# Kernel optimization log

Measured on AMD Instinct MI355X. Metric: run time of the kernel, lower is better.

## Reference

```python
import jax, jax.numpy as jnp
import numpy as np

XBOUND = (-51.2, 51.2, 0.8)
YBOUND = (-51.2, 51.2, 0.8)
ZBOUND = (-10.0, 10.0, 20.0)
DBOUND = (1.0, 60.0, 1.0)
IMG_H, IMG_W = 256, 704
DOWNSAMPLE = 16
CAM_C = 64
OUT_C = 64
D = int((DBOUND[1] - DBOUND[0]) / DBOUND[2])      # 59
NX = int((XBOUND[1] - XBOUND[0]) / XBOUND[2])     # 128
NY = int((YBOUND[1] - YBOUND[0]) / YBOUND[2])     # 128
NZ = int((ZBOUND[1] - ZBOUND[0]) / ZBOUND[2])     # 1
FH, FW = IMG_H // DOWNSAMPLE, IMG_W // DOWNSAMPLE # 16, 44
DX = jnp.array([XBOUND[2], YBOUND[2], ZBOUND[2]], dtype=jnp.float32)
BX = jnp.array([XBOUND[0] + XBOUND[2] / 2.0, YBOUND[0] + YBOUND[2] / 2.0, ZBOUND[0] + ZBOUND[2] / 2.0], dtype=jnp.float32)


def make_frustum():
    ds = jnp.arange(DBOUND[0], DBOUND[1], DBOUND[2], dtype=jnp.float32)   # [D]
    xs = jnp.linspace(0.0, IMG_W - 1.0, FW, dtype=jnp.float32)            # [FW]
    ys = jnp.linspace(0.0, IMG_H - 1.0, FH, dtype=jnp.float32)            # [FH]
    d = jnp.broadcast_to(ds[:, None, None], (D, FH, FW))
    x = jnp.broadcast_to(xs[None, None, :], (D, FH, FW))
    y = jnp.broadcast_to(ys[None, :, None], (D, FH, FW))
    return jnp.stack([x, y, d], axis=-1)                                  # [D,FH,FW,3]


def get_geometry(rots, trans, intrins, post_rots, post_trans):
    # rots/intrins/post_rots: [B,N,3,3]; trans/post_trans: [B,N,3]
    frustum = make_frustum()                                              # [D,FH,FW,3]
    pts = frustum[None, None] - post_trans[:, :, None, None, None]        # [B,N,D,FH,FW,3]
    pts = jnp.einsum('bnij,bndhwj->bndhwi', jnp.linalg.inv(post_rots), pts)
    pts = jnp.concatenate([pts[..., :2] * pts[..., 2:3], pts[..., 2:3]], axis=-1)
    comb = jnp.matmul(rots, jnp.linalg.inv(intrins))
    pts = jnp.einsum('bnij,bndhwj->bndhwi', comb, pts)
    return pts + trans[:, :, None, None, None]


def forward(x, rots, trans, intrins, post_rots, post_trans, w_depth, b_depth):
    B, N, C_in, H, W = x.shape
    # 1x1 conv == channel matmul
    y = jnp.einsum('bnchw,oc->bnohw', x, w_depth) + b_depth[None, None, :, None, None]
    depth = jax.nn.softmax(y[:, :, :D], axis=2)              # [B,N,D,H,W]
    context = y[:, :, D:]                                    # [B,N,OUT_C,H,W]
    outer = depth[:, :, :, None] * context[:, :, None, :]    # [B,N,D,OUT_C,H,W]
    outer = jnp.transpose(outer, (0, 1, 2, 4, 5, 3))         # [B,N,D,H,W,OUT_C]

    geom = jax.lax.stop_gradient(get_geometry(rots, trans, intrins, post_rots, post_trans))
    # torch .long() truncates toward zero -> jnp.trunc
    g = jnp.trunc((geom.reshape(-1, 3) - (BX - DX / 2.0)) / DX).astype(jnp.int32)  # [P,3]
    kept = ((g[:, 0] >= 0) & (g[:, 0] < NX) &
            (g[:, 1] >= 0) & (g[:, 1] < NY) &
            (g[:, 2] >= 0) & (g[:, 2] < NZ))
    batch_ix = jnp.repeat(jnp.arange(B, dtype=jnp.int32), N * D * H * W)
    ranks = batch_ix * (NX * NY * NZ) + g[:, 0] + g[:, 1] * NX + g[:, 2] * NX * NY
    # segment-sum over voxel ranks == sort+cumsum trick + scatter in the original
    feats = jnp.where(kept[:, None], outer.reshape(-1, OUT_C), 0.0)
    ranks = jnp.where(kept, ranks, 0)
    bev = jax.ops.segment_sum(feats, ranks, num_segments=B * NZ * NY * NX)
    bev = bev.reshape(B, NZ, NY, NX, OUT_C).transpose(0, 4, 1, 2, 3).sum(axis=2)
    return bev  # [B, OUT_C, NY, NX]


def setup_inputs() -> dict:
    key = jax.random.key(0)
    B, N = 4, 6
    ks = jax.random.split(key, 8)
    cam2ego = jnp.array([[0.0, 0.0, 1.0], [-1.0, 0.0, 0.0], [0.0, -1.0, 0.0]], dtype=jnp.float32)
    rots = jnp.broadcast_to(cam2ego, (B, N, 3, 3)) + 0.02 * jax.random.normal(ks[0], (B, N, 3, 3), dtype=jnp.float32)
    trans = 1.0 * jax.random.normal(ks[1], (B, N, 3), dtype=jnp.float32)
    K = jnp.array([[700.0, 0.0, IMG_W / 2.0], [0.0, 700.0, IMG_H / 2.0], [0.0, 0.0, 1.0]], dtype=jnp.float32)
    intrins = jnp.broadcast_to(K, (B, N, 3, 3)) + 0.1 * jax.random.normal(ks[2], (B, N, 3, 3), dtype=jnp.float32)
    post_rots = jnp.broadcast_to(jnp.eye(3, dtype=jnp.float32), (B, N, 3, 3)) + 0.01 * jax.random.normal(ks[3], (B, N, 3, 3), dtype=jnp.float32)
    post_trans = 0.1 * jax.random.normal(ks[4], (B, N, 3), dtype=jnp.float32)
    x = jax.random.normal(ks[5], (B, N, CAM_C, FH, FW), dtype=jnp.float32)
    w_depth = 0.05 * jax.random.normal(ks[6], (D + OUT_C, CAM_C), dtype=jnp.float32)
    b_depth = jnp.zeros((D + OUT_C,), dtype=jnp.float32)
    return {"x": x, "rots": rots, "trans": trans, "intrins": intrins,
            "post_rots": post_rots, "post_trans": post_trans,
            "w_depth": w_depth, "b_depth": b_depth}


def reference(x, rots, trans, intrins, post_rots, post_trans, w_depth, b_depth):
    return forward(x, rots, trans, intrins, post_rots, post_trans, w_depth, b_depth)
```

## Files before the change

kernel.cpp:

```cpp
#include <hip/hip_runtime.h>
#include <math.h>

#define Bc 4
#define Nc 6
#define Dc 59
#define FHc 16
#define FWc 44
#define Cc 64
#define OCc 123
#define NXc 128
#define NYc 128
#define NVOX (Bc*NXc*NYc)
#define NBLK (Bc*Nc*FWc)
#define NBLK2 (NBLK*2)

#define WS_ACC 0
#define WS_CAM ((size_t)16777216)
#define WS_WDT ((size_t)16781312)

template<bool FMA>
__device__ __forceinline__ float mulsub(float a, float b, float c) {
    if (FMA) return __fmaf_rn(-a, b, c);
    return __fadd_rn(c, __fmul_rn(-a, b));
}

template<bool FMA>
__device__ __forceinline__ void lu_inv3x3T(const float* __restrict__ m, float* __restrict__ o) {
    float A[3][3] = {{m[0],m[3],m[6]},{m[1],m[4],m[7]},{m[2],m[5],m[8]}};
    int piv0, piv1;
    {
        float a0=fabsf(A[0][0]), a1=fabsf(A[1][0]), a2=fabsf(A[2][0]);
        int p = 0; float mx = a0;
        if (a1 > mx) { mx = a1; p = 1; }
        if (a2 > mx) { mx = a2; p = 2; }
        piv0 = p;
        if (p != 0) { for (int k=0;k<3;++k){ float t=A[0][k]; A[0][k]=A[p][k]; A[p][k]=t; } }
        const float d = __fdiv_rn(1.0f, A[0][0]);
        A[1][0] = __fmul_rn(A[1][0], d);
        A[2][0] = __fmul_rn(A[2][0], d);
        #pragma unroll
        for (int i=1;i<3;++i)
            #pragma unroll
            for (int j=1;j<3;++j)
                A[i][j] = mulsub<FMA>(A[i][0], A[0][j], A[i][j]);
    }
    {
        float a1=fabsf(A[1][1]), a2=fabsf(A[2][1]);
        int p = (a2 > a1) ? 2 : 1;
        piv1 = p;
        if (p != 1) { for (int k=0;k<3;++k){ float t=A[1][k]; A[1][k]=A[p][k]; A[p][k]=t; } }
        const float d = __fdiv_rn(1.0f, A[1][1]);
        A[2][1] = __fmul_rn(A[2][1], d);
        A[2][2] = mulsub<FMA>(A[2][1], A[1][2], A[2][2]);
    }
    float B[3][3] = {{1.f,0.f,0.f},{0.f,1.f,0.f},{0.f,0.f,1.f}};
    if (piv0 != 0) { for (int k=0;k<3;++k){ float t=B[0][k]; B[0][k]=B[piv0][k]; B[piv0][k]=t; } }
    if (piv1 != 1) { for (int k=0;k<3;++k){ float t=B[1][k]; B[1][k]=B[piv1][k]; B[piv1][k]=t; } }
    #pragma unroll
    for (int j=0;j<3;++j) {
        B[1][j] = mulsub<FMA>(A[1][0], B[0][j], B[1][j]);
        B[2][j] = mulsub<FMA>(A[2][0], B[0][j], B[2][j]);
        B[2][j] = mulsub<FMA>(A[2][1], B[1][j], B[2][j]);
        B[2][j] = __fdiv_rn(B[2][j], A[2][2]);
        B[0][j] = mulsub<FMA>(A[0][2], B[2][j], B[0][j]);
        B[1][j] = mulsub<FMA>(A[1][2], B[2][j], B[1][j]);
        B[1][j] = __fdiv_rn(B[1][j], A[1][1]);
        B[0][j] = mulsub<FMA>(A[0][1], B[1][j], B[0][j]);
        B[0][j] = __fdiv_rn(B[0][j], A[0][0]);
    }
    o[0]=B[0][0]; o[1]=B[1][0]; o[2]=B[2][0];
    o[3]=B[0][1]; o[4]=B[1][1]; o[5]=B[2][1];
    o[6]=B[0][2]; o[7]=B[1][2]; o[8]=B[2][2];
}

template<bool FMA>
__device__ __forceinline__ float dot3(float a0,float a1,float a2,float b0,float b1,float b2){
    if (FMA) return __fmaf_rn(a2,b2, __fmaf_rn(a1,b1, __fmul_rn(a0,b0)));
    return __fadd_rn(__fadd_rn(__fmul_rn(a0,b0), __fmul_rn(a1,b1)), __fmul_rn(a2,b2));
}

__global__ __launch_bounds__(256) void prep(
    const float* __restrict__ wd, const float* __restrict__ rots,
    const float* __restrict__ intrins, const float* __restrict__ post_rots,
    float* __restrict__ wdT2, float* __restrict__ camMat, float4* __restrict__ acc4)
{
    const int gid = blockIdx.x*256 + threadIdx.x;
    const float4 z = make_float4(0.f, 0.f, 0.f, 0.f);
    acc4[gid] = z;
    acc4[gid + 524288] = z;

    if (gid < OCc*Cc) {
        const int o = gid >> 6, c = gid & 63;
        const int slot = (o < 64) ? (o << 1) : (((o - 64) << 1) | 1);
        wdT2[(c << 7) + slot] = wd[gid];
    } else if (gid < OCc*Cc + 320) {
        const int k = gid - OCc*Cc;
        const int c = k / 5, o = 59 + (k % 5);
        wdT2[(c << 7) + (o << 1) + 1] = 0.0f;
    }
    if (gid < 48) {
        const int cam = gid >> 1;
        const int var = gid & 1;
        const float* pr = post_rots + cam*9;
        const float* ro = rots      + cam*9;
        const float* it = intrins   + cam*9;
        float PRi[9], INi[9], CM[9];
        if (var == 0) { lu_inv3x3T<true >(pr, PRi); lu_inv3x3T<true >(it, INi); }
        else          { lu_inv3x3T<false>(pr, PRi); lu_inv3x3T<false>(it, INi); }
        #pragma unroll
        for (int r2 = 0; r2 < 3; ++r2)
            #pragma unroll
            for (int c2 = 0; c2 < 3; ++c2)
                CM[r2*3+c2] = dot3<true>(ro[r2*3+0], ro[r2*3+1], ro[r2*3+2],
                                         INi[0*3+c2], INi[1*3+c2], INi[2*3+c2]);
        float* dst = camMat + (size_t)(cam*2 + var)*18;
        #pragma unroll
        for (int k = 0; k < 9; ++k) { dst[k] = PRi[k]; dst[9+k] = CM[k]; }
    }
}

template<bool FMA>
__device__ __forceinline__ int geom_light(
    const float* __restrict__ PRi, const float* __restrict__ CM,
    float pt0, float pt1, float pt2, float tr0, float tr1, float tr2,
    float u, float v, float dval, int b)
{
    const float p0 = __fsub_rn(u,    pt0);
    const float p1 = __fsub_rn(v,    pt1);
    const float p2 = __fsub_rn(dval, pt2);
    const float q0 = dot3<FMA>(PRi[0],PRi[1],PRi[2], p0,p1,p2);
    const float q1 = dot3<FMA>(PRi[3],PRi[4],PRi[5], p0,p1,p2);
    const float q2 = dot3<FMA>(PRi[6],PRi[7],PRi[8], p0,p1,p2);
    const float r0 = __fmul_rn(q0, q2);
    const float r1 = __fmul_rn(q1, q2);
    const float s0 = __fadd_rn(dot3<FMA>(CM[0],CM[1],CM[2], r0,r1,q2), tr0);
    const float s1 = __fadd_rn(dot3<FMA>(CM[3],CM[4],CM[5], r0,r1,q2), tr1);
    const float s2 = __fadd_rn(dot3<FMA>(CM[6],CM[7],CM[8], r0,r1,q2), tr2);
    const float CX  = -51.200000762939453f;
    const float DXf =  0.80000001192092896f;
    const float gx = __fdiv_rn(__fsub_rn(s0, CX), DXf);
    const float gy = __fdiv_rn(__fsub_rn(s1, CX), DXf);
    const float gz = __fdiv_rn(__fsub_rn(s2, -10.0f), 20.0f);
    const bool kept = (gx > -1.0f) && (gx < 128.0f) &&
                      (gy > -1.0f) && (gy < 128.0f) &&
                      (gz > -1.0f) && (gz < 1.0f);
    return kept ? (b*(NXc*NYc) + ((int)gy)*NXc + (int)gx) : -1;
}

__global__ __launch_bounds__(256, 8) void lss_main(
    const float* __restrict__ x, const float* __restrict__ trans,
    const float* __restrict__ post_trans, const float* __restrict__ bd,
    const float* __restrict__ wdT2, const float* __restrict__ camMat,
    float* __restrict__ acc)
{
    const int blk2 = blockIdx.x;
    const int pixblk = blk2 >> 1;
    const int half = blk2 & 1;
    const int d0 = half * 30;
    const int dn = 30 - half;
    const int wi  = pixblk % FWc;
    const int cam = pixblk / FWc;
    const int b   = cam / Nc;
    const int t = threadIdx.x;
    const int wave = t >> 6, lane = t & 63;

    __shared__ float  xsT[64][16];
    __shared__ float  yv[16][60];
    __shared__ float  ctxT[64][18];
    __shared__ float4 geo[30][16];

    {
        const float* xb = x + (size_t)cam*64*(FHc*FWc) + wi;
        for (int idx = t; idx < 1024; idx += 256) {
            const int c = idx >> 4, hi = idx & 15;
            xsT[c][hi] = xb[(size_t)c*(FHc*FWc) + hi*FWc];
        }
    }
    __syncthreads();

    {
        const int hi0 = wave << 2;
        float a0[4] = {0.f,0.f,0.f,0.f}, a1[4] = {0.f,0.f,0.f,0.f};
        const float2* wrow = (const float2*)wdT2 + lane;
        #pragma unroll 8
        for (int c = 0; c < 64; ++c) {
            const float2 wv = wrow[c << 6];
            const float4 xv = *(const float4*)&xsT[c][hi0];
            a0[0] = __fmaf_rn(wv.x, xv.x, a0[0]); a1[0] = __fmaf_rn(wv.y, xv.x, a1[0]);
            a0[1] = __fmaf_rn(wv.x, xv.y, a0[1]); a1[1] = __fmaf_rn(wv.y, xv.y, a1[1]);
            a0[2] = __fmaf_rn(wv.x, xv.z, a0[2]); a1[2] = __fmaf_rn(wv.y, xv.z, a1[2]);
            a0[3] = __fmaf_rn(wv.x, xv.w, a0[3]); a1[3] = __fmaf_rn(wv.y, xv.w, a1[3]);
        }
        const float b0 = bd[lane];
        const float b1 = (lane < 59) ? bd[64 + lane] : 0.0f;
        #pragma unroll
        for (int k = 0; k < 4; ++k) {
            const int hi = hi0 + k;
            const float y0 = __fadd_rn(a0[k], b0);
            if (lane < 59) {
                yv[hi][lane] = y0;
                ctxT[lane + 5][hi] = __fadd_rn(a1[k], b1);
            } else {
                ctxT[lane - 59][hi] = y0;
            }
        }
    }
    for (int k = 0; k < 4; ++k) {
        const int hi = (wave << 2) | k;
        float v = (lane < Dc) ? yv[hi][lane] : -INFINITY;
        float m = v;
        #pragma unroll
        for (int off = 32; off; off >>= 1) m = fmaxf(m, __shfl_xor(m, off));
        float e = (lane < Dc) ? expf(__fsub_rn(v, m)) : 0.0f;
        float s = e;
        #pragma unroll
        for (int off = 32; off; off >>= 1) s = __fadd_rn(s, __shfl_xor(s, off));
        if (lane < Dc) yv[hi][lane] = __fdiv_rn(e, s);
    }
    __syncthreads();

    {
        const float pt0 = post_trans[cam*3+0], pt1 = post_trans[cam*3+1], pt2 = post_trans[cam*3+2];
        const float tr0 = trans[cam*3+0],      tr1 = trans[cam*3+1],      tr2 = trans[cam*3+2];
        const float* M0 = camMat + (size_t)(cam*2 + 0)*18;
        const float* M1 = camMat + (size_t)(cam*2 + 1)*18;
        const float u = (float)(wi * (703.0 / 43.0));
        for (int idx = t; idx < 16*dn; idx += 256) {
            const int dd = idx >> 4, hi = idx & 15;
            const int d = d0 + dd;
            const float v    = (float)(hi * 17.0);
            const float dval = (float)(1 + d);
            const int vA = geom_light<true >(M0, M0+9, pt0,pt1,pt2, tr0,tr1,tr2, u, v, dval, b);
            const int vB = geom_light<false>(M1, M1+9, pt0,pt1,pt2, tr0,tr1,tr2, u, v, dval, b);
            geo[dd][hi] = make_float4(yv[hi][d], __int_as_float(vA), __int_as_float(vB), 0.0f);
        }
    }
    __syncthreads();

    {
        float cx[16];
        #pragma unroll
        for (int h = 0; h < 16; h += 2) {
            const float2 c2 = *(const float2*)&ctxT[lane][h];
            cx[h] = c2.x; cx[h+1] = c2.y;
        }
        for (int dd = wave; dd < dn; dd += 4) {
            int runVox = -1;
            float accv = 0.0f;
            #pragma unroll
            for (int hi = 0; hi < 16; ++hi) {
                const float4 g = geo[dd][hi];
                const float dw = g.x;
                const int vA = __float_as_int(g.y);
                const int vB = __float_as_int(g.z);
                const float cxv = cx[hi];
                if (vA == vB) {
                    if (vA >= 0) {
                        if (vA != runVox) {
                            if (runVox >= 0) atomicAdd(&acc[((size_t)runVox << 6) + lane], accv);
                            runVox = vA; accv = 0.0f;
                        }
                        accv = __fadd_rn(accv, __fmul_rn(dw, cxv));
                    }
                } else {
                    const float hw = __fmul_rn(dw, 0.5f);
                    if (vA >= 0) {
                        if (vA != runVox) {
                            if (runVox >= 0) atomicAdd(&acc[((size_t)runVox << 6) + lane], accv);
                            runVox = vA; accv = 0.0f;
                        }
                        accv = __fadd_rn(accv, __fmul_rn(hw, cxv));
                    }
                    if (vB >= 0) atomicAdd(&acc[((size_t)vB << 6) + lane], __fmul_rn(hw, cxv));
                }
            }
            if (runVox >= 0) atomicAdd(&acc[((size_t)runVox << 6) + lane], accv);
        }
    }
}

__global__ __launch_bounds__(256) void lss_transpose(
    const float* __restrict__ acc, float* __restrict__ out)
{
    __shared__ float tile[64][65];
    const int blk = blockIdx.x;
    const int b = blk >> 8;
    const int pixbase = (blk & 255) * 64;
    const float4* src4 = (const float4*)(acc + ((size_t)b*16384 + pixbase)*64);
    const int t = threadIdx.x;
    #pragma unroll
    for (int i = 0; i < 4; ++i) {
        const int e4 = i*256 + t;
        const float4 v = src4[e4];
        const int e = e4 << 2;
        const int r = e & 63, c = e >> 6;
        tile[r+0][c] = v.x; tile[r+1][c] = v.y; tile[r+2][c] = v.z; tile[r+3][c] = v.w;
    }
    __syncthreads();
    float* dst = out + (size_t)b*64*16384 + pixbase;
    #pragma unroll
    for (int i = 0; i < 4; ++i) {
        const int idx = i*256 + t;
        const int c = idx >> 4, p = (idx & 15) << 2;
        const float4 v = make_float4(tile[c][p], tile[c][p+1], tile[c][p+2], tile[c][p+3]);
        *(float4*)&dst[(size_t)c*16384 + p] = v;
    }
}

extern "C" void kernel_launch(void* const* d_in, const int* in_sizes, int n_in,
                              void* d_out, int out_size, void* d_ws, size_t ws_size,
                              hipStream_t stream) {
    const float* x          = (const float*)d_in[0];
    const float* rots       = (const float*)d_in[1];
    const float* trans      = (const float*)d_in[2];
    const float* intrins    = (const float*)d_in[3];
    const float* post_rots  = (const float*)d_in[4];
    const float* post_trans = (const float*)d_in[5];
    const float* wd         = (const float*)d_in[6];
    const float* bd         = (const float*)d_in[7];
    float* out = (float*)d_out;
    char* ws = (char*)d_ws;

    float* acc    = (float*)(ws + WS_ACC);
    float* camMat = (float*)(ws + WS_CAM);
    float* wdT2   = (float*)(ws + WS_WDT);

    prep<<<dim3(2048), dim3(256), 0, stream>>>(
        wd, rots, intrins, post_rots, wdT2, camMat, (float4*)acc);
    lss_main<<<dim3(NBLK2), dim3(256), 0, stream>>>(
        x, trans, post_trans, bd, wdT2, camMat, acc);
    lss_transpose<<<dim3(Bc*256), dim3(256), 0, stream>>>(acc, out);
}
```

Measured before the change: 220.0 us.

## Merge depth-split blocks into single 512-thread block per pixel column

Each pixel column (camera, width index) was previously handled by two 256-thread blocks, each covering half the depth bins, and each recomputing the x load, 1x1 conv and softmax. Now one 512-thread block covers all 59 depth bins, so the conv and softmax run once per column and are spread over 8 waves instead of 4. This removes the duplicated conv and softmax work, but halves the grid to 1056 blocks and enlarges shared memory for the geometry table, which may lower occupancy and parallelism.

```diff
diff --git a/kernel.cpp b/kernel.cpp
--- a/kernel.cpp
+++ b/kernel.cpp
@@ -12,7 +12,6 @@
 #define NYc 128
 #define NVOX (Bc*NXc*NYc)
 #define NBLK (Bc*Nc*FWc)
-#define NBLK2 (NBLK*2)
 
 #define WS_ACC 0
 #define WS_CAM ((size_t)16777216)
@@ -147,19 +146,15 @@
     return kept ? (b*(NXc*NYc) + ((int)gy)*NXc + (int)gx) : -1;
 }
 
-__global__ __launch_bounds__(256, 8) void lss_main(
+__global__ __launch_bounds__(512, 8) void lss_main(
     const float* __restrict__ x, const float* __restrict__ trans,
     const float* __restrict__ post_trans, const float* __restrict__ bd,
     const float* __restrict__ wdT2, const float* __restrict__ camMat,
     float* __restrict__ acc)
 {
-    const int blk2 = blockIdx.x;
-    const int pixblk = blk2 >> 1;
-    const int half = blk2 & 1;
-    const int d0 = half * 30;
-    const int dn = 30 - half;
-    const int wi  = pixblk % FWc;
-    const int cam = pixblk / FWc;
+    const int blk = blockIdx.x;
+    const int wi  = blk % FWc;
+    const int cam = blk / FWc;
     const int b   = cam / Nc;
     const int t = threadIdx.x;
     const int wave = t >> 6, lane = t & 63;
@@ -167,11 +162,11 @@
     __shared__ float  xsT[64][16];
     __shared__ float  yv[16][60];
     __shared__ float  ctxT[64][18];
-    __shared__ float4 geo[30][16];
+    __shared__ float4 geo[Dc][16];
 
     {
         const float* xb = x + (size_t)cam*64*(FHc*FWc) + wi;
-        for (int idx = t; idx < 1024; idx += 256) {
+        for (int idx = t; idx < 1024; idx += 512) {
             const int c = idx >> 4, hi = idx & 15;
             xsT[c][hi] = xb[(size_t)c*(FHc*FWc) + hi*FWc];
         }
@@ -179,22 +174,20 @@
     __syncthreads();
 
     {
-        const int hi0 = wave << 2;
-        float a0[4] = {0.f,0.f,0.f,0.f}, a1[4] = {0.f,0.f,0.f,0.f};
+        const int hi0 = wave << 1;
+        float a0[2] = {0.f,0.f}, a1[2] = {0.f,0.f};
         const float2* wrow = (const float2*)wdT2 + lane;
         #pragma unroll 8
         for (int c = 0; c < 64; ++c) {
             const float2 wv = wrow[c << 6];
-            const float4 xv = *(const float4*)&xsT[c][hi0];
+            const float2 xv = *(const float2*)&xsT[c][hi0];
             a0[0] = __fmaf_rn(wv.x, xv.x, a0[0]); a1[0] = __fmaf_rn(wv.y, xv.x, a1[0]);
             a0[1] = __fmaf_rn(wv.x, xv.y, a0[1]); a1[1] = __fmaf_rn(wv.y, xv.y, a1[1]);
-            a0[2] = __fmaf_rn(wv.x, xv.z, a0[2]); a1[2] = __fmaf_rn(wv.y, xv.z, a1[2]);
-            a0[3] = __fmaf_rn(wv.x, xv.w, a0[3]); a1[3] = __fmaf_rn(wv.y, xv.w, a1[3]);
         }
         const float b0 = bd[lane];
         const float b1 = (lane < 59) ? bd[64 + lane] : 0.0f;
         #pragma unroll
-        for (int k = 0; k < 4; ++k) {
+        for (int k = 0; k < 2; ++k) {
             const int hi = hi0 + k;
             const float y0 = __fadd_rn(a0[k], b0);
             if (lane < 59) {
@@ -205,8 +198,8 @@
             }
         }
     }
-    for (int k = 0; k < 4; ++k) {
-        const int hi = (wave << 2) | k;
+    for (int k = 0; k < 2; ++k) {
+        const int hi = (wave << 1) | k;
         float v = (lane < Dc) ? yv[hi][lane] : -INFINITY;
         float m = v;
         #pragma unroll
@@ -225,14 +218,13 @@
         const float* M0 = camMat + (size_t)(cam*2 + 0)*18;
         const float* M1 = camMat + (size_t)(cam*2 + 1)*18;
         const float u = (float)(wi * (703.0 / 43.0));
-        for (int idx = t; idx < 16*dn; idx += 256) {
-            const int dd = idx >> 4, hi = idx & 15;
-            const int d = d0 + dd;
+        for (int idx = t; idx < 16*Dc; idx += 512) {
+            const int d = idx >> 4, hi = idx & 15;
             const float v    = (float)(hi * 17.0);
             const float dval = (float)(1 + d);
             const int vA = geom_light<true >(M0, M0+9, pt0,pt1,pt2, tr0,tr1,tr2, u, v, dval, b);
             const int vB = geom_light<false>(M1, M1+9, pt0,pt1,pt2, tr0,tr1,tr2, u, v, dval, b);
-            geo[dd][hi] = make_float4(yv[hi][d], __int_as_float(vA), __int_as_float(vB), 0.0f);
+            geo[d][hi] = make_float4(yv[hi][d], __int_as_float(vA), __int_as_float(vB), 0.0f);
         }
     }
     __syncthreads();
@@ -244,12 +236,12 @@
             const float2 c2 = *(const float2*)&ctxT[lane][h];
             cx[h] = c2.x; cx[h+1] = c2.y;
         }
-        for (int dd = wave; dd < dn; dd += 4) {
+        for (int d = wave; d < Dc; d += 8) {
             int runVox = -1;
             float accv = 0.0f;
             #pragma unroll
             for (int hi = 0; hi < 16; ++hi) {
-                const float4 g = geo[dd][hi];
+                const float4 g = geo[d][hi];
                 const float dw = g.x;
                 const int vA = __float_as_int(g.y);
                 const int vB = __float_as_int(g.z);
@@ -327,7 +319,7 @@
 
     prep<<<dim3(2048), dim3(256), 0, stream>>>(
         wd, rots, intrins, post_rots, wdT2, camMat, (float4*)acc);
-    lss_main<<<dim3(NBLK2), dim3(256), 0, stream>>>(
+    lss_main<<<dim3(NBLK), dim3(512), 0, stream>>>(
         x, trans, post_trans, bd, wdT2, camMat, acc);
     lss_transpose<<<dim3(Bc*256), dim3(256), 0, stream>>>(acc, out);
 }
```

New measurement: 185.0 us. -15.9%, faster.
